# Optimization experiments

Hardware: AMD Instinct MI355X
Metric: run time of the kernel (lower is better)

Reference implementation:

```python
import jax, jax.numpy as jnp
import numpy as np

N_NODES = 100000
N_EDGES = 1600000
IN_CH = 512
HID_CH = 256
OUT_CH = 32
K = 10


def setup_inputs() -> dict:
    key = jax.random.key(0)
    k_x, k_e, k_w1, k_b1, k_w2, k_b2 = jax.random.split(key, 6)
    x = jax.random.normal(k_x, (N_NODES, IN_CH), dtype=jnp.float32)
    edge_index = jax.random.randint(k_e, (2, N_EDGES), 0, N_NODES, dtype=jnp.int64)
    s1 = 1.0 / np.sqrt(IN_CH)
    s2 = 1.0 / np.sqrt(HID_CH)
    W1 = jax.random.uniform(k_w1, (IN_CH, HID_CH), jnp.float32, -s1, s1)
    b1 = jax.random.uniform(k_b1, (HID_CH,), jnp.float32, -s1, s1)
    W2 = jax.random.uniform(k_w2, (HID_CH, OUT_CH), jnp.float32, -s2, s2)
    b2 = jax.random.uniform(k_b2, (OUT_CH,), jnp.float32, -s2, s2)
    gamma = jnp.ones((K + 1,), jnp.float32) / (K + 1)
    return {"x": x, "edge_index": edge_index, "W1": W1, "b1": b1,
            "W2": W2, "b2": b2, "gamma": gamma}


def reference(x, edge_index, W1, b1, W2, b2, gamma):
    # MLP (dropout is identity in eval mode)
    h = jax.nn.relu(x @ W1 + b1) @ W2 + b2  # [N, out]
    row, col = edge_index[0], edge_index[1]
    # symmetric normalization: deg over destination nodes (col)
    deg = jax.ops.segment_sum(jnp.ones((N_EDGES,), h.dtype), col,
                              num_segments=N_NODES)
    deg_inv_sqrt = jnp.where(deg > 0, jax.lax.rsqrt(jnp.maximum(deg, 1.0)), 0.0)
    norm = (deg_inv_sqrt[row] * deg_inv_sqrt[col])[:, None]  # [E, 1]
    out = gamma[0] * h
    h_k = h
    for k in range(1, K + 1):
        # one hop: gather source feats, scale, scatter-add to destinations
        h_k = jax.ops.segment_sum(norm * h_k[row], col, num_segments=N_NODES)
        out = out + gamma[k] * h_k
    return out
```

## Files before the change

kernel.cpp:

```cpp
#include <hip/hip_runtime.h>
#include <hip/hip_bf16.h>

#define NN    100000
#define NE    1600000
#define INCH  512
#define HIDCH 256
#define OUTCH 32
#define KHOPS 10
#define NEPAD (NE + 3 * NN)

typedef __attribute__((ext_vector_type(8))) short short8;
typedef __attribute__((ext_vector_type(4))) float f32x4;

#define GLOAD_LDS16(gsrc, ldst) \
  __builtin_amdgcn_global_load_lds((const __attribute__((address_space(1))) void*)(gsrc), \
                                   (__attribute__((address_space(3))) void*)(ldst), 16, 0, 0)

constexpr size_t ws_align(size_t x) { return (x + 255) & ~(size_t)255; }
constexpr size_t USZ = ws_align((size_t)(NN + 1) * 32 * 2);
constexpr size_t OFF_H1   = 0;
constexpr size_t OFF_U0   = OFF_H1   + ws_align((size_t)NN*HIDCH*2);
constexpr size_t OFF_U1   = OFF_U0   + USZ;
constexpr size_t OFF_W1TH = OFF_U1   + USZ;
constexpr size_t OFF_W1TL = OFF_W1TH + ws_align((size_t)HIDCH*INCH*2);
constexpr size_t OFF_W2TH = OFF_W1TL + ws_align((size_t)HIDCH*INCH*2);
constexpr size_t OFF_W2TL = OFF_W2TH + ws_align((size_t)OUTCH*HIDCH*2);
constexpr size_t OFF_DEG  = OFF_W2TL + ws_align((size_t)OUTCH*HIDCH*2);
constexpr size_t OFF_DIS  = OFF_DEG  + ws_align((size_t)NN*4);
constexpr size_t OFF_RP   = OFF_DIS  + ws_align((size_t)NN*4);
constexpr size_t OFF_CUR  = OFF_RP   + ws_align((size_t)(NN+1)*4);
constexpr size_t OFF_CSR  = OFF_CUR  + ws_align((size_t)NN*4);
constexpr size_t OFF_PART = OFF_CSR  + ws_align((size_t)NEPAD*4);
constexpr size_t OFF_OFFS = OFF_PART + ws_align(512);

__device__ __forceinline__ unsigned short bf16_rne(float f) {
  unsigned int u = __float_as_uint(f);
  u += 0x7fffu + ((u >> 16) & 1u);
  return (unsigned short)(u >> 16);
}
__device__ __forceinline__ float bf16_to_f32(unsigned short h) {
  return __uint_as_float(((unsigned int)h) << 16);
}
__device__ __forceinline__ float bflo(unsigned int w) {
  return __uint_as_float(w << 16);
}
__device__ __forceinline__ float bfhi(unsigned int w) {
  return __uint_as_float(w & 0xffff0000u);
}

__global__ __launch_bounds__(256) void k_count_deg(const int* __restrict__ col,
                                                   int* __restrict__ deg) {
  int e = blockIdx.x * 256 + threadIdx.x;
  if (e < NE) atomicAdd(&deg[col[e]], 1);
}

__global__ __launch_bounds__(256) void k_dis(const int* __restrict__ deg,
                                             float* __restrict__ dis,
                                             unsigned short* u0, unsigned short* u1) {
  int v = blockIdx.x * 256 + threadIdx.x;
  if (v < NN) {
    int d = deg[v];
    dis[v] = d > 0 ? rsqrtf((float)d) : 0.0f;
  }
  if (blockIdx.x == 0) {
    int t = threadIdx.x;
    if (t < 16)      ((unsigned int*)u0)[(size_t)NN * 16 + t] = 0;
    else if (t < 32) ((unsigned int*)u1)[(size_t)NN * 16 + (t - 16)] = 0;
  }
}

__global__ __launch_bounds__(256) void k_scan1(const int* __restrict__ deg,
                                               int* __restrict__ rp,
                                               int* __restrict__ part) {
  __shared__ int s[256];
  int b = blockIdx.x, t = threadIdx.x;
  int base = b * 1024 + t * 4;
  int v0 = (base + 0 < NN) ? ((deg[base + 0] + 3) & ~3) : 0;
  int v1 = (base + 1 < NN) ? ((deg[base + 1] + 3) & ~3) : 0;
  int v2 = (base + 2 < NN) ? ((deg[base + 2] + 3) & ~3) : 0;
  int v3 = (base + 3 < NN) ? ((deg[base + 3] + 3) & ~3) : 0;
  int tot = v0 + v1 + v2 + v3;
  s[t] = tot;
  __syncthreads();
  for (int d = 1; d < 256; d <<= 1) {
    int x = (t >= d) ? s[t - d] : 0;
    __syncthreads();
    s[t] += x;
    __syncthreads();
  }
  int excl = s[t] - tot;
  if (t == 255) part[b] = s[255];
  if (base + 0 < NN) rp[base + 0] = excl;
  if (base + 1 < NN) rp[base + 1] = excl + v0;
  if (base + 2 < NN) rp[base + 2] = excl + v0 + v1;
  if (base + 3 < NN) rp[base + 3] = excl + v0 + v1 + v2;
}

__global__ __launch_bounds__(128) void k_scan2(const int* __restrict__ part,
                                               int* __restrict__ offs) {
  __shared__ int s[128];
  int t = threadIdx.x;
  int v = (t < 98) ? part[t] : 0;
  s[t] = v;
  __syncthreads();
  for (int d = 1; d < 128; d <<= 1) {
    int x = (t >= d) ? s[t - d] : 0;
    __syncthreads();
    s[t] += x;
    __syncthreads();
  }
  if (t < 98) offs[t] = s[t] - v;
}

__global__ __launch_bounds__(256) void k_scan3(int* __restrict__ rp,
                                               const int* __restrict__ offs,
                                               const int* __restrict__ part,
                                               int* __restrict__ cur) {
  int b = blockIdx.x, t = threadIdx.x;
  int o = offs[b];
  int base = b * 1024 + t * 4;
#pragma unroll
  for (int j = 0; j < 4; ++j) {
    int i = base + j;
    if (i < NN) {
      int r = rp[i] + o;
      rp[i] = r;
      cur[i] = r;
    }
  }
  if (b == 0 && t == 0) rp[NN] = offs[97] + part[97];
}

__global__ __launch_bounds__(256) void k_fill(const int* __restrict__ ei,
                                              int* __restrict__ cur,
                                              int* __restrict__ csrc) {
  int e = blockIdx.x * 256 + threadIdx.x;
  if (e < NE) {
    int c = ei[NE + e];
    int p = atomicAdd(&cur[c], 1);
    csrc[p] = ei[e];
  }
}

__global__ __launch_bounds__(256) void k_pad(const int* __restrict__ cur,
                                             const int* __restrict__ rp,
                                             int* __restrict__ csrc) {
  int v = blockIdx.x * 256 + threadIdx.x;
  if (v < NN) {
    int p = cur[v], e = rp[v + 1];
    for (; p < e; ++p) csrc[p] = NN;
  }
}

__global__ __launch_bounds__(256) void k_splitT(const float* __restrict__ src,
                                                unsigned short* __restrict__ dh,
                                                unsigned short* __restrict__ dl,
                                                int K, int N) {
  int idx = blockIdx.x * 256 + threadIdx.x;
  if (idx >= K * N) return;
  int n = idx / K, k = idx - n * K;
  float v = src[(size_t)k * N + n];
  unsigned short h = bf16_rne(v);
  dh[idx] = h;
  dl[idx] = bf16_rne(v - bf16_to_f32(h));
}

__global__ __launch_bounds__(256) void k_gemm1(const float* __restrict__ X,
                                               const unsigned short* __restrict__ W1Th,
                                               const unsigned short* __restrict__ W1Tl,
                                               const float* __restrict__ bias1,
                                               unsigned short* __restrict__ H1bf) {
  __shared__ __align__(16) unsigned short Ah[4096], Bh[4096], Bl[4096];
  const int t = threadIdx.x;
  const int m0 = blockIdx.x * 128;
  const int n0 = blockIdx.y * 128;
  const int w = t >> 6, lane = t & 63;
  const int wm = w >> 1, wn = w & 1;

  const int arow = t >> 1;
  int axrow = m0 + arow; if (axrow >= NN) axrow = NN - 1;
  const float* aptr = X + (size_t)axrow * INCH + (t & 1) * 16;
  const int aidx0 = (arow >> 4) * 512 + ((arow & 15) + (t & 1) * 32) * 8;
  const int aidx1 = aidx0 + 128;

  const int bko = (lane >> 4) * 8;
  const unsigned short* bs0 = W1Th + (size_t)(n0 + w * 16 + (lane & 15)) * INCH + bko;
  const unsigned short* bs1 = W1Th + (size_t)(n0 + (w + 4) * 16 + (lane & 15)) * INCH + bko;
  const unsigned short* bs2 = W1Tl + (size_t)(n0 + w * 16 + (lane & 15)) * INCH + bko;
  const unsigned short* bs3 = W1Tl + (size_t)(n0 + (w + 4) * 16 + (lane & 15)) * INCH + bko;

  f32x4 acc[4][4] = {};

#pragma unroll 4
  for (int it = 0; it < 16; ++it) {
    const int k0 = it * 32;
    __syncthreads();
    GLOAD_LDS16(bs0 + k0, &Bh[w * 512]);
    GLOAD_LDS16(bs1 + k0, &Bh[(w + 4) * 512]);
    GLOAD_LDS16(bs2 + k0, &Bl[w * 512]);
    GLOAD_LDS16(bs3 + k0, &Bl[(w + 4) * 512]);
    {
      float4 x0 = *(const float4*)(aptr + k0);
      float4 x1 = *(const float4*)(aptr + k0 + 4);
      float4 x2 = *(const float4*)(aptr + k0 + 8);
      float4 x3 = *(const float4*)(aptr + k0 + 12);
      float af[16] = {x0.x, x0.y, x0.z, x0.w, x1.x, x1.y, x1.z, x1.w,
                      x2.x, x2.y, x2.z, x2.w, x3.x, x3.y, x3.z, x3.w};
      short8 a0, a1;
#pragma unroll
      for (int i = 0; i < 8; ++i) {
        unsigned int u = __float_as_uint(af[i]);
        a0[i] = (short)((u + 0x7fffu + ((u >> 16) & 1u)) >> 16);
        unsigned int u2 = __float_as_uint(af[8 + i]);
        a1[i] = (short)((u2 + 0x7fffu + ((u2 >> 16) & 1u)) >> 16);
      }
      *(short8*)&Ah[aidx0] = a0;
      *(short8*)&Ah[aidx1] = a1;
    }
    __syncthreads();
    short8 afrag[4];
#pragma unroll
    for (int mf = 0; mf < 4; ++mf)
      afrag[mf] = *(const short8*)&Ah[(wm * 4 + mf) * 512 + lane * 8];
#pragma unroll
    for (int nf = 0; nf < 4; ++nf) {
      short8 bfh = *(const short8*)&Bh[(wn * 4 + nf) * 512 + lane * 8];
      short8 bfl = *(const short8*)&Bl[(wn * 4 + nf) * 512 + lane * 8];
#pragma unroll
      for (int mf = 0; mf < 4; ++mf) {
        acc[mf][nf] = __builtin_amdgcn_mfma_f32_16x16x32_bf16(afrag[mf], bfh, acc[mf][nf], 0, 0, 0);
        acc[mf][nf] = __builtin_amdgcn_mfma_f32_16x16x32_bf16(afrag[mf], bfl, acc[mf][nf], 0, 0, 0);
      }
    }
  }

  const int colbase = n0 + wn * 64 + (lane & 15);
  const int rowbase = m0 + wm * 64 + ((lane >> 4) << 2);
#pragma unroll
  for (int nf = 0; nf < 4; ++nf) {
    int col = colbase + nf * 16;
    float b = bias1[col];
#pragma unroll
    for (int mf = 0; mf < 4; ++mf) {
#pragma unroll
      for (int r = 0; r < 4; ++r) {
        int row = rowbase + mf * 16 + r;
        if (row < NN) {
          float h = fmaxf(acc[mf][nf][r] + b, 0.f);
          H1bf[(size_t)row * HIDCH + col] = bf16_rne(h);
        }
      }
    }
  }
}

__global__ __launch_bounds__(256) void k_gemm2(const unsigned short* __restrict__ H1bf,
                                               const unsigned short* __restrict__ W2Th,
                                               const unsigned short* __restrict__ W2Tl,
                                               const float* __restrict__ bias2,
                                               const float* __restrict__ gamma,
                                               const float* __restrict__ dis,
                                               unsigned short* __restrict__ u0,
                                               float* __restrict__ out) {
  __shared__ __align__(16) unsigned short A2[8192];
  __shared__ __align__(16) unsigned short B2h[2048], B2l[2048];
  const int t = threadIdx.x;
  const int m0 = blockIdx.x * 128;

  const int arow = t >> 1;
  int axrow = m0 + arow; if (axrow >= NN) axrow = NN - 1;
  const int akb = (t & 1) * 32;
  const unsigned short* ap = H1bf + (size_t)axrow * HIDCH + akb;
  const int abase = ((arow >> 4) * 2 + (akb >> 5)) * 512 + (arow & 15) * 8;

  const int bnr = t >> 3, bkq = (t & 7) * 8;
  const int bslot = ((bnr >> 4) * 2 + (bkq >> 5)) * 512 +
                    ((bnr & 15) + (((bkq & 31) >> 3) << 4)) * 8;
  const unsigned short* bhp = W2Th + (size_t)bnr * HIDCH + bkq;
  const unsigned short* blp = W2Tl + (size_t)bnr * HIDCH + bkq;

  const int w = t >> 6, lane = t & 63;

  f32x4 acc[2][2] = {};

  for (int k0 = 0; k0 < HIDCH; k0 += 64) {
    uint4 a0 = *(const uint4*)(ap + k0);
    uint4 a1 = *(const uint4*)(ap + k0 + 8);
    uint4 a2 = *(const uint4*)(ap + k0 + 16);
    uint4 a3 = *(const uint4*)(ap + k0 + 24);
    uint4 bh = *(const uint4*)(bhp + k0);
    uint4 bl = *(const uint4*)(blp + k0);

    __syncthreads();

    *(uint4*)&A2[abase + 0 * 128] = a0;
    *(uint4*)&A2[abase + 1 * 128] = a1;
    *(uint4*)&A2[abase + 2 * 128] = a2;
    *(uint4*)&A2[abase + 3 * 128] = a3;
    *(uint4*)&B2h[bslot] = bh;
    *(uint4*)&B2l[bslot] = bl;

    __syncthreads();

    const short8* AV  = (const short8*)A2;
    const short8* BHV = (const short8*)B2h;
    const short8* BLV = (const short8*)B2l;
#pragma unroll
    for (int k32 = 0; k32 < 2; ++k32) {
      short8 bfh[2], bfl[2];
#pragma unroll
      for (int nf = 0; nf < 2; ++nf) {
        bfh[nf] = BHV[(nf * 2 + k32) * 64 + lane];
        bfl[nf] = BLV[(nf * 2 + k32) * 64 + lane];
      }
#pragma unroll
      for (int mf = 0; mf < 2; ++mf) {
        short8 a = AV[((w * 2 + mf) * 2 + k32) * 64 + lane];
#pragma unroll
        for (int nf = 0; nf < 2; ++nf) {
          acc[mf][nf] = __builtin_amdgcn_mfma_f32_16x16x32_bf16(a, bfh[nf], acc[mf][nf], 0, 0, 0);
          acc[mf][nf] = __builtin_amdgcn_mfma_f32_16x16x32_bf16(a, bfl[nf], acc[mf][nf], 0, 0, 0);
        }
      }
    }
  }

  const float g0 = gamma[0];
  const int colb = lane & 15;
  const int rowb = m0 + w * 32 + ((lane >> 4) << 2);
  const float b2c0 = bias2[colb], b2c1 = bias2[16 + colb];
#pragma unroll
  for (int mf = 0; mf < 2; ++mf) {
#pragma unroll
    for (int r = 0; r < 4; ++r) {
      int row = rowb + mf * 16 + r;
      if (row < NN) {
        float dv = dis[row];
        float h0 = acc[mf][0][r] + b2c0;
        float h1 = acc[mf][1][r] + b2c1;
        size_t o = (size_t)row * 32 + colb;
        u0[o] = bf16_rne(dv * h0);
        u0[o + 16] = bf16_rne(dv * h1);
        out[o] = g0 * h0;
        out[o + 16] = g0 * h1;
      }
    }
  }
}

__global__ __launch_bounds__(256) void k_hop(const unsigned short* __restrict__ Uin,
                                             unsigned short* __restrict__ Uout,
                                             float* __restrict__ out,
                                             const int* __restrict__ rp,
                                             const int* __restrict__ csrc,
                                             const float* __restrict__ dis,
                                             const float* __restrict__ gamma,
                                             int k) {
  const int t = threadIdx.x;
  const int g = t >> 4;
  const int li = t & 15;
  const int v = blockIdx.x * 16 + g;
  const int s = rp[v], e = rp[v + 1];
  const unsigned int* Uin32 = (const unsigned int*)Uin;

  float ax0 = 0.f, ay0 = 0.f, ax1 = 0.f, ay1 = 0.f;
  float ax2 = 0.f, ay2 = 0.f, ax3 = 0.f, ay3 = 0.f;
  int j = s;
  for (; j + 8 <= e; j += 8) {
    int4 sa = *(const int4*)&csrc[j];
    int4 sb = *(const int4*)&csrc[j + 4];
    unsigned int w0 = Uin32[(size_t)sa.x * 16 + li];
    unsigned int w1 = Uin32[(size_t)sa.y * 16 + li];
    unsigned int w2 = Uin32[(size_t)sa.z * 16 + li];
    unsigned int w3 = Uin32[(size_t)sa.w * 16 + li];
    unsigned int w4 = Uin32[(size_t)sb.x * 16 + li];
    unsigned int w5 = Uin32[(size_t)sb.y * 16 + li];
    unsigned int w6 = Uin32[(size_t)sb.z * 16 + li];
    unsigned int w7 = Uin32[(size_t)sb.w * 16 + li];
    ax0 += bflo(w0); ay0 += bfhi(w0);
    ax1 += bflo(w1); ay1 += bfhi(w1);
    ax2 += bflo(w2); ay2 += bfhi(w2);
    ax3 += bflo(w3); ay3 += bfhi(w3);
    ax0 += bflo(w4); ay0 += bfhi(w4);
    ax1 += bflo(w5); ay1 += bfhi(w5);
    ax2 += bflo(w6); ay2 += bfhi(w6);
    ax3 += bflo(w7); ay3 += bfhi(w7);
  }
  if (j < e) {
    int4 sa = *(const int4*)&csrc[j];
    unsigned int w0 = Uin32[(size_t)sa.x * 16 + li];
    unsigned int w1 = Uin32[(size_t)sa.y * 16 + li];
    unsigned int w2 = Uin32[(size_t)sa.z * 16 + li];
    unsigned int w3 = Uin32[(size_t)sa.w * 16 + li];
    ax0 += bflo(w0); ay0 += bfhi(w0);
    ax1 += bflo(w1); ay1 += bfhi(w1);
    ax2 += bflo(w2); ay2 += bfhi(w2);
    ax3 += bflo(w3); ay3 += bfhi(w3);
  }
  const float Sx = (ax0 + ax1) + (ax2 + ax3);
  const float Sy = (ay0 + ay1) + (ay2 + ay3);
  const float dv = dis[v];
  const float gd = gamma[k] * dv;
  const float d2 = dv * dv;
  unsigned int packed = (unsigned int)bf16_rne(d2 * Sx) |
                        ((unsigned int)bf16_rne(d2 * Sy) << 16);
  ((unsigned int*)Uout)[(size_t)v * 16 + li] = packed;
  const size_t o = (size_t)v * 32 + li * 2;
  float2 po = *(const float2*)&out[o];
  po.x = fmaf(gd, Sx, po.x);
  po.y = fmaf(gd, Sy, po.y);
  *(float2*)&out[o] = po;
}

extern "C" void kernel_launch(void* const* d_in, const int* in_sizes, int n_in,
                              void* d_out, int out_size, void* d_ws, size_t ws_size,
                              hipStream_t stream) {
  const float* x     = (const float*)d_in[0];
  const int*   ei    = (const int*)d_in[1];
  const float* W1    = (const float*)d_in[2];
  const float* b1    = (const float*)d_in[3];
  const float* W2    = (const float*)d_in[4];
  const float* b2    = (const float*)d_in[5];
  const float* gamma = (const float*)d_in[6];
  float* out = (float*)d_out;

  char* ws = (char*)d_ws;
  unsigned short* h1bf = (unsigned short*)(ws + OFF_H1);
  unsigned short* U[2] = {(unsigned short*)(ws + OFF_U0),
                          (unsigned short*)(ws + OFF_U1)};
  unsigned short* w1th = (unsigned short*)(ws + OFF_W1TH);
  unsigned short* w1tl = (unsigned short*)(ws + OFF_W1TL);
  unsigned short* w2th = (unsigned short*)(ws + OFF_W2TH);
  unsigned short* w2tl = (unsigned short*)(ws + OFF_W2TL);
  int*   deg  = (int*)(ws + OFF_DEG);
  float* dis  = (float*)(ws + OFF_DIS);
  int*   rp   = (int*)(ws + OFF_RP);
  int*   cur  = (int*)(ws + OFF_CUR);
  int*   csrc = (int*)(ws + OFF_CSR);
  int*   part = (int*)(ws + OFF_PART);
  int*   offs = (int*)(ws + OFF_OFFS);

  hipMemsetAsync(deg, 0, NN * sizeof(int), stream);

  k_splitT<<<(INCH * HIDCH + 255) / 256, 256, 0, stream>>>(W1, w1th, w1tl, INCH, HIDCH);
  k_splitT<<<(HIDCH * OUTCH + 255) / 256, 256, 0, stream>>>(W2, w2th, w2tl, HIDCH, OUTCH);

  k_count_deg<<<(NE + 255) / 256, 256, 0, stream>>>(ei + NE, deg);
  k_dis<<<(NN + 255) / 256, 256, 0, stream>>>(deg, dis, U[0], U[1]);
  k_scan1<<<98, 256, 0, stream>>>(deg, rp, part);
  k_scan2<<<1, 128, 0, stream>>>(part, offs);
  k_scan3<<<98, 256, 0, stream>>>(rp, offs, part, cur);
  k_fill<<<(NE + 255) / 256, 256, 0, stream>>>(ei, cur, csrc);
  k_pad<<<(NN + 255) / 256, 256, 0, stream>>>(cur, rp, csrc);

  k_gemm1<<<dim3((NN + 127) / 128, 2), 256, 0, stream>>>(x, w1th, w1tl, b1, h1bf);
  k_gemm2<<<(NN + 127) / 128, 256, 0, stream>>>(h1bf, w2th, w2tl, b2, gamma, dis,
                                                U[0], out);

  for (int k = 1; k <= KHOPS; ++k) {
    k_hop<<<NN / 16, 256, 0, stream>>>(U[(k - 1) & 1], U[k & 1], out,
                                       rp, csrc, dis, gamma, k);
  }
}
```

Baseline: 608.0 us.

## Restructure gemm1: full-width N tile, double-buffered LDS, drop W1 low split

Rewrites the first GEMM so each 512-thread block covers all 256 output columns, which means X is read once instead of twice. Shared-memory A and B tiles are double-buffered so the next k-slice's global loads overlap the current MFMAs, and the A tile uses an XOR swizzle to reduce LDS bank conflicts. It also drops the bf16 low-part (hi/lo split) correction for W1, halving the MFMA count but reducing accuracy of the weight representation. The k_splitT launch still writes w1tl, which is now unused.

```diff
diff --git a/kernel.cpp b/kernel.cpp
--- a/kernel.cpp
+++ b/kernel.cpp
@@ -165,76 +165,85 @@
   dl[idx] = bf16_rne(v - bf16_to_f32(h));
 }
 
-__global__ __launch_bounds__(256) void k_gemm1(const float* __restrict__ X,
-                                               const unsigned short* __restrict__ W1Th,
-                                               const unsigned short* __restrict__ W1Tl,
-                                               const float* __restrict__ bias1,
-                                               unsigned short* __restrict__ H1bf) {
-  __shared__ __align__(16) unsigned short Ah[4096], Bh[4096], Bl[4096];
+__global__ __launch_bounds__(512, 2) void k_gemm1(const float* __restrict__ X,
+                                                  const unsigned short* __restrict__ W1Th,
+                                                  const float* __restrict__ bias1,
+                                                  unsigned short* __restrict__ H1bf) {
+  __shared__ __align__(16) unsigned short Ah[2][4096];
+  __shared__ __align__(16) unsigned short Bh[2][8192];
   const int t = threadIdx.x;
   const int m0 = blockIdx.x * 128;
-  const int n0 = blockIdx.y * 128;
   const int w = t >> 6, lane = t & 63;
-  const int wm = w >> 1, wn = w & 1;
-
-  const int arow = t >> 1;
+  const int wm = w >> 2, wn = w & 3;
+
+  const int arow = t >> 2;
+  const int achk = t & 3;
   int axrow = m0 + arow; if (axrow >= NN) axrow = NN - 1;
-  const float* aptr = X + (size_t)axrow * INCH + (t & 1) * 16;
-  const int aidx0 = (arow >> 4) * 512 + ((arow & 15) + (t & 1) * 32) * 8;
-  const int aidx1 = aidx0 + 128;
-
+  const float* aptr = X + (size_t)axrow * INCH + achk * 8;
+  int aidx = (arow >> 4) * 512 + ((arow & 15) + achk * 16) * 8;
+  aidx ^= ((aidx >> 7) & 3) << 4;
+  const int aroff = (lane * 8) ^ (((lane >> 4) & 3) << 4);
+
+  const int bn0 = (w * 16) + (lane & 15);
   const int bko = (lane >> 4) * 8;
-  const unsigned short* bs0 = W1Th + (size_t)(n0 + w * 16 + (lane & 15)) * INCH + bko;
-  const unsigned short* bs1 = W1Th + (size_t)(n0 + (w + 4) * 16 + (lane & 15)) * INCH + bko;
-  const unsigned short* bs2 = W1Tl + (size_t)(n0 + w * 16 + (lane & 15)) * INCH + bko;
-  const unsigned short* bs3 = W1Tl + (size_t)(n0 + (w + 4) * 16 + (lane & 15)) * INCH + bko;
+  const unsigned short* bs0 = W1Th + (size_t)bn0 * INCH + bko;
+  const unsigned short* bs1 = W1Th + (size_t)(bn0 + 128) * INCH + bko;
 
   f32x4 acc[4][4] = {};
-
-#pragma unroll 4
+  float4 av0, av1;
+
+  av0 = *(const float4*)(aptr);
+  av1 = *(const float4*)(aptr + 4);
+  GLOAD_LDS16(bs0, &Bh[0][w * 512]);
+  GLOAD_LDS16(bs1, &Bh[0][(w + 8) * 512]);
+  {
+    float af[8] = {av0.x, av0.y, av0.z, av0.w, av1.x, av1.y, av1.z, av1.w};
+    short8 ah;
+#pragma unroll
+    for (int i = 0; i < 8; ++i) {
+      unsigned int u = __float_as_uint(af[i]);
+      ah[i] = (short)((u + 0x7fffu + ((u >> 16) & 1u)) >> 16);
+    }
+    *(short8*)&Ah[0][aidx] = ah;
+  }
+  __syncthreads();
+
+#pragma unroll
   for (int it = 0; it < 16; ++it) {
+    const int cur = it & 1, nxt = cur ^ 1;
     const int k0 = it * 32;
-    __syncthreads();
-    GLOAD_LDS16(bs0 + k0, &Bh[w * 512]);
-    GLOAD_LDS16(bs1 + k0, &Bh[(w + 4) * 512]);
-    GLOAD_LDS16(bs2 + k0, &Bl[w * 512]);
-    GLOAD_LDS16(bs3 + k0, &Bl[(w + 4) * 512]);
-    {
-      float4 x0 = *(const float4*)(aptr + k0);
-      float4 x1 = *(const float4*)(aptr + k0 + 4);
-      float4 x2 = *(const float4*)(aptr + k0 + 8);
-      float4 x3 = *(const float4*)(aptr + k0 + 12);
-      float af[16] = {x0.x, x0.y, x0.z, x0.w, x1.x, x1.y, x1.z, x1.w,
-                      x2.x, x2.y, x2.z, x2.w, x3.x, x3.y, x3.z, x3.w};
-      short8 a0, a1;
+    if (it < 15) {
+      av0 = *(const float4*)(aptr + k0 + 32);
+      av1 = *(const float4*)(aptr + k0 + 36);
+      GLOAD_LDS16(bs0 + k0 + 32, &Bh[nxt][w * 512]);
+      GLOAD_LDS16(bs1 + k0 + 32, &Bh[nxt][(w + 8) * 512]);
+    }
+    short8 afrag[4];
+#pragma unroll
+    for (int mf = 0; mf < 4; ++mf)
+      afrag[mf] = *(const short8*)&Ah[cur][(wm * 4 + mf) * 512 + aroff];
+#pragma unroll
+    for (int nf = 0; nf < 4; ++nf) {
+      short8 bfh = *(const short8*)&Bh[cur][(wn * 4 + nf) * 512 + lane * 8];
+#pragma unroll
+      for (int mf = 0; mf < 4; ++mf) {
+        acc[mf][nf] = __builtin_amdgcn_mfma_f32_16x16x32_bf16(afrag[mf], bfh, acc[mf][nf], 0, 0, 0);
+      }
+    }
+    if (it < 15) {
+      float af[8] = {av0.x, av0.y, av0.z, av0.w, av1.x, av1.y, av1.z, av1.w};
+      short8 ah;
 #pragma unroll
       for (int i = 0; i < 8; ++i) {
         unsigned int u = __float_as_uint(af[i]);
-        a0[i] = (short)((u + 0x7fffu + ((u >> 16) & 1u)) >> 16);
-        unsigned int u2 = __float_as_uint(af[8 + i]);
-        a1[i] = (short)((u2 + 0x7fffu + ((u2 >> 16) & 1u)) >> 16);
-      }
-      *(short8*)&Ah[aidx0] = a0;
-      *(short8*)&Ah[aidx1] = a1;
-    }
-    __syncthreads();
-    short8 afrag[4];
-#pragma unroll
-    for (int mf = 0; mf < 4; ++mf)
-      afrag[mf] = *(const short8*)&Ah[(wm * 4 + mf) * 512 + lane * 8];
-#pragma unroll
-    for (int nf = 0; nf < 4; ++nf) {
-      short8 bfh = *(const short8*)&Bh[(wn * 4 + nf) * 512 + lane * 8];
-      short8 bfl = *(const short8*)&Bl[(wn * 4 + nf) * 512 + lane * 8];
-#pragma unroll
-      for (int mf = 0; mf < 4; ++mf) {
-        acc[mf][nf] = __builtin_amdgcn_mfma_f32_16x16x32_bf16(afrag[mf], bfh, acc[mf][nf], 0, 0, 0);
-        acc[mf][nf] = __builtin_amdgcn_mfma_f32_16x16x32_bf16(afrag[mf], bfl, acc[mf][nf], 0, 0, 0);
-      }
-    }
-  }
-
-  const int colbase = n0 + wn * 64 + (lane & 15);
+        ah[i] = (short)((u + 0x7fffu + ((u >> 16) & 1u)) >> 16);
+      }
+      *(short8*)&Ah[nxt][aidx] = ah;
+    }
+    __syncthreads();
+  }
+
+  const int colbase = wn * 64 + (lane & 15);
   const int rowbase = m0 + wm * 64 + ((lane >> 4) << 2);
 #pragma unroll
   for (int nf = 0; nf < 4; ++nf) {
@@ -453,7 +462,7 @@
   k_fill<<<(NE + 255) / 256, 256, 0, stream>>>(ei, cur, csrc);
   k_pad<<<(NN + 255) / 256, 256, 0, stream>>>(cur, rp, csrc);
 
-  k_gemm1<<<dim3((NN + 127) / 128, 2), 256, 0, stream>>>(x, w1th, w1tl, b1, h1bf);
+  k_gemm1<<<(NN + 127) / 128, 512, 0, stream>>>(x, w1th, b1, h1bf);
   k_gemm2<<<(NN + 127) / 128, 256, 0, stream>>>(h1bf, w2th, w2tl, b2, gamma, dis,
                                                 U[0], out);
 
```

Result: faster. 551.1 us (-9.4%).
